# Kernel tuning notes

Measured on AMD Instinct MI355X. Metric: run time of the kernel, lower is better.

## Reference

```python
import jax, jax.numpy as jnp
import numpy as np

B, N, F_DIM = 64, 4096, 64
K_SLOTS, D, N_ITERS = 8, 64, 3
EPS = 1e-8
LN_EPS = 1e-5  # torch LayerNorm default


def layernorm(x, g, b):
    mu = jnp.mean(x, axis=-1, keepdims=True)
    var = jnp.mean(jnp.square(x - mu), axis=-1, keepdims=True)
    return (x - mu) * jax.lax.rsqrt(var + LN_EPS) * g + b


def gru_cell(x, h, w_ih, w_hh, b_ih, b_hh):
    # torch.nn.GRUCell semantics; weights are [3D, D] with gate order r, z, n
    gi = x @ w_ih.T + b_ih
    gh = h @ w_hh.T + b_hh
    i_r, i_z, i_n = jnp.split(gi, 3, axis=-1)
    h_r, h_z, h_n = jnp.split(gh, 3, axis=-1)
    r = jax.nn.sigmoid(i_r + h_r)
    z = jax.nn.sigmoid(i_z + h_z)
    n = jnp.tanh(i_n + r * h_n)
    return (1.0 - z) * n + z * h


def setup_inputs() -> dict:
    key = jax.random.key(0)
    ks = jax.random.split(key, 16)
    f32 = jnp.float32
    s = 0.05  # small init scale for weights
    return {
        "inputs": jax.random.normal(ks[0], (B, N, F_DIM), f32),
        "slots_noise": jax.random.normal(ks[1], (B, K_SLOTS, D), f32),
        "slots_mu": jax.random.normal(ks[2], (1, 1, D), f32) * s,
        "slots_log_sigma": jax.random.normal(ks[3], (1, 1, D), f32) * s,
        "Wq": jax.random.normal(ks[4], (D, D), f32) * s,
        "Wk": jax.random.normal(ks[5], (D, F_DIM), f32) * s,
        "Wv": jax.random.normal(ks[6], (D, F_DIM), f32) * s,
        "gru_w_ih": jax.random.normal(ks[7], (3 * D, D), f32) * s,
        "gru_w_hh": jax.random.normal(ks[8], (3 * D, D), f32) * s,
        "gru_b_ih": jnp.zeros((3 * D,), f32),
        "gru_b_hh": jnp.zeros((3 * D,), f32),
        "mlp_w1": jax.random.normal(ks[9], (2 * D, D), f32) * s,
        "mlp_b1": jnp.zeros((2 * D,), f32),
        "mlp_w2": jax.random.normal(ks[10], (D, 2 * D), f32) * s,
        "mlp_b2": jnp.zeros((D,), f32),
        "ln_in_g": jnp.ones((F_DIM,), f32), "ln_in_b": jnp.zeros((F_DIM,), f32),
        "ln_slots_g": jnp.ones((D,), f32), "ln_slots_b": jnp.zeros((D,), f32),
        "ln_mlp_g": jnp.ones((D,), f32), "ln_mlp_b": jnp.zeros((D,), f32),
    }


def reference(inputs, slots_noise, slots_mu, slots_log_sigma, Wq, Wk, Wv,
              gru_w_ih, gru_w_hh, gru_b_ih, gru_b_hh,
              mlp_w1, mlp_b1, mlp_w2, mlp_b2,
              ln_in_g, ln_in_b, ln_slots_g, ln_slots_b, ln_mlp_g, ln_mlp_b):
    x = layernorm(inputs, ln_in_g, ln_in_b)          # [B, N, F]
    k = jnp.einsum('bnf,df->bnd', x, Wk)             # [B, N, D]
    v = jnp.einsum('bnf,df->bnd', x, Wv)             # [B, N, D]

    slots = slots_mu + jnp.exp(slots_log_sigma) * slots_noise  # [B, K, D]
    scale = D ** -0.5

    for _ in range(N_ITERS):
        slots_prev = slots
        s_n = layernorm(slots, ln_slots_g, ln_slots_b)
        q = jnp.einsum('bkd,ed->bke', s_n, Wq)                  # [B, K, D]
        attn_logits = jnp.einsum('bnd,bkd->bnk', k, q) * scale  # [B, N, K]
        attn = jax.nn.softmax(attn_logits, axis=-1) + EPS       # softmax over slots
        attn = attn / jnp.sum(attn, axis=1, keepdims=True)      # renormalize over N
        updates = jnp.einsum('bnk,bnd->bkd', attn, v)           # [B, K, D]
        slots = gru_cell(updates.reshape(-1, D), slots_prev.reshape(-1, D),
                         gru_w_ih, gru_w_hh, gru_b_ih, gru_b_hh).reshape(B, K_SLOTS, D)
        h = layernorm(slots, ln_mlp_g, ln_mlp_b)
        h = jax.nn.relu(h @ mlp_w1.T + mlp_b1) @ mlp_w2.T + mlp_b2
        slots = slots + h
    return slots
```

## Files before the change

### kernel.cpp

```cpp
#include <hip/hip_runtime.h>
#include <math.h>

#define NN 4096
#define LN_EPS 1e-5f
#define EPS 1e-8f

typedef unsigned short ushortT;
typedef unsigned int uintT;
typedef __attribute__((ext_vector_type(8))) short short8;
typedef __attribute__((ext_vector_type(4))) float f32x4;
typedef __attribute__((ext_vector_type(2))) float f32x2;
typedef __attribute__((ext_vector_type(4))) unsigned short us4;

#define OFF_QU    0L
#define OFF_AP    98304L
#define OFF_CP    884736L
#define OFF_SLOTS 897024L
#define OFF_WIHT  995328L
#define OFF_WHHT  1007616L
#define OFF_W1T   1019904L
#define OFF_W2T   1028096L
#define OFF_WQT   1036288L
#define OFF_WVT   1040384L
#define OFF_CNT   1044480L
#define OFF_RDY   1044672L

__device__ __forceinline__ float wredsum(float v) {
#pragma unroll
  for (int off = 32; off > 0; off >>= 1) v += __shfl_xor(v, off);
  return v;
}

__device__ __forceinline__ ushortT f2bf(float f) {
  uintT b = __float_as_uint(f);
  b += 0x7fff + ((b >> 16) & 1);
  return (ushortT)(b >> 16);
}

__device__ __forceinline__ uintT pack2bf(float lo, float hi) {
  return (uintT)f2bf(lo) | ((uintT)f2bf(hi) << 16);
}

__device__ __forceinline__ void store2_coh(float* p, f32x2 v) {
  asm volatile("global_store_dwordx2 %0, %1, off sc0 sc1" :: "v"(p), "v"(v) : "memory");
}
__device__ __forceinline__ void store1f_coh(float* p, float v) {
  asm volatile("global_store_dword %0, %1, off sc0 sc1" :: "v"(p), "v"(v) : "memory");
}
__device__ __forceinline__ void store1u_coh(uintT* p, uintT v) {
  asm volatile("global_store_dword %0, %1, off sc0 sc1" :: "v"(p), "v"(v) : "memory");
}
__device__ __forceinline__ uintT load1u_coh(const uintT* p) {
  uintT r;
  asm volatile("global_load_dword %0, %1, off sc0 sc1\n\t"
               "s_waitcnt vmcnt(0)" : "=v"(r) : "v"(p) : "memory");
  return r;
}
__device__ __forceinline__ void drain_vm() {
  asm volatile("s_waitcnt vmcnt(0)" ::: "memory");
}
__device__ __forceinline__ void wait_lds() {
  asm volatile("s_waitcnt lgkmcnt(0)" ::: "memory");
}

__global__ __launch_bounds__(256) void k_prep(
    const float* __restrict__ w_ih, const float* __restrict__ w_hh,
    const float* __restrict__ w1, const float* __restrict__ w2,
    const float* __restrict__ Wq, const float* __restrict__ Wv,
    const float* __restrict__ Wk,
    const float* __restrict__ noise, const float* __restrict__ smu,
    const float* __restrict__ slsig,
    const float* __restrict__ g_sl, const float* __restrict__ b_sl,
    float* __restrict__ wihT, float* __restrict__ whhT,
    float* __restrict__ w1T, float* __restrict__ w2T, float* __restrict__ wqT,
    float* __restrict__ wvT, float* __restrict__ slotsV, uintT* __restrict__ qU,
    uintT* __restrict__ cnt, uintT* __restrict__ ready)
{
  const int tid = threadIdx.x;
  if (blockIdx.x >= 194) {
    __shared__ float SI[4][192];
    const int lane = tid & 63, wave = tid >> 6;
    const int bi = blockIdx.x - 194;
    const int row = bi * 4 + wave;
    const int b = row >> 3, ks = row & 7;
    float* Sw = SI[wave];

    float s0 = fmaf(expf(slsig[lane]), noise[row * 64 + lane], smu[lane]);
    slotsV[row * 64 + lane] = s0;

    float mu = wredsum(s0) * (1.f / 64.f);
    float dx = s0 - mu;
    float var = wredsum(dx * dx) * (1.f / 64.f);
    float sn = dx * rsqrtf(var + LN_EPS) * g_sl[lane] + b_sl[lane];
    Sw[lane] = sn;
    float qe = 0.f;
#pragma unroll 16
    for (int d = 0; d < 64; ++d) qe = fmaf(Sw[d], Wq[lane * 64 + d], qe);
    Sw[64 + lane] = qe;
    float qp = 0.f;
#pragma unroll 16
    for (int e = 0; e < 64; ++e) qp = fmaf(Sw[64 + e], Wk[e * 64 + lane], qp);
    Sw[128 + lane] = qp * 0.125f;
    if (lane < 32) {
      const int kb = lane >> 4, lrow = (lane >> 2) & 3, j2 = lane & 3;
      const int fA = kb * 32 + lrow * 8 + 2 * j2;
      uintT u = pack2bf(Sw[128 + fA], Sw[128 + fA + 1]);
      qU[((b * 2 + kb) * 64 + lrow * 16 + ks) * 4 + j2] = u;
#pragma unroll
      for (int v = 0; v < 3; ++v)
        qU[v * 32768 + ((b * 2 + kb) * 64 + lrow * 16 + 8 + ks) * 4 + j2] = 0u;
    }
    return;
  }

  int idx = blockIdx.x * 256 + tid;
  if (idx < 12288) {
    int j = idx >> 6, f = idx & 63;
    wihT[f * 192 + j] = w_ih[idx];
  } else if (idx < 24576) {
    int i = idx - 12288; int j = i >> 6, f = i & 63;
    whhT[f * 192 + j] = w_hh[i];
  } else if (idx < 32768) {
    int i = idx - 24576; int j = i >> 6, f = i & 63;
    w1T[f * 128 + j] = w1[i];
  } else if (idx < 40960) {
    int i = idx - 32768; int d = i >> 7, j = i & 127;
    w2T[j * 64 + d] = w2[i];
  } else if (idx < 45056) {
    int i = idx - 40960; int e = i >> 6, d = i & 63;
    wqT[d * 64 + e] = Wq[i];
  } else if (idx < 49152) {
    int i = idx - 45056; int d = i >> 6, f = i & 63;
    wvT[f * 64 + d] = Wv[i];
  } else if (idx < 49344) {
    cnt[idx - 49152] = 0u;
  } else if (idx < 49408) {
    ready[idx - 49344] = 0u;
  }
}

__global__ __launch_bounds__(256, 2) void k_attn(
    const float* __restrict__ inp,
    const float* __restrict__ g_in, const float* __restrict__ b_in,
    uintT* __restrict__ qU,
    float* __restrict__ accPart, float* __restrict__ colPart,
    uintT* __restrict__ cnt, uintT* __restrict__ ready,
    float* __restrict__ slotsV,
    const float* __restrict__ wihT, const float* __restrict__ whhT,
    const float* __restrict__ w1T, const float* __restrict__ w2T,
    const float* __restrict__ wqT, const float* __restrict__ Wk,
    const float* __restrict__ wvT,
    const float* __restrict__ b_ih, const float* __restrict__ b_hh,
    const float* __restrict__ mb1, const float* __restrict__ mb2,
    const float* __restrict__ g_ml, const float* __restrict__ b_ml,
    const float* __restrict__ g_sl, const float* __restrict__ b_sl,
    float* __restrict__ dout)
{
  __shared__ __align__(16) ushortT XW[4][4096];
  __shared__ int lastFlag;
  const int tid = threadIdx.x;
  const int lane = tid & 63;
  const int wave = tid >> 6;
  const int l15 = lane & 15, q = lane >> 4;
  const int b = blockIdx.x >> 3;
  const int e = blockIdx.x & 7;

  ushortT* xT = &XW[wave][0];

  short8 kA0[4][2], kA1[4][2];
  {
    const float4 g4 = *(const float4*)&g_in[l15 << 2];
    const float4 b4 = *(const float4*)&b_in[l15 << 2];
#pragma unroll
    for (int ch = 0; ch < 2; ++ch) {
      const int chunk = (e << 3) + (ch << 2) + wave;
      const float* rowbase = inp + (((long)b * NN + (chunk << 6)) << 6);
#pragma unroll
      for (int pass = 0; pass < 16; ++pass) {
        const int row = (pass << 2) + q;
        float4 x = *(const float4*)&rowbase[(row << 6) + (l15 << 2)];
        float s = x.x + x.y + x.z + x.w;
        s += __shfl_xor(s, 1); s += __shfl_xor(s, 2);
        s += __shfl_xor(s, 4); s += __shfl_xor(s, 8);
        const float mu = s * (1.f / 64.f);
        float4 dx = {x.x - mu, x.y - mu, x.z - mu, x.w - mu};
        float ss = dx.x * dx.x + dx.y * dx.y + dx.z * dx.z + dx.w * dx.w;
        ss += __shfl_xor(ss, 1); ss += __shfl_xor(ss, 2);
        ss += __shfl_xor(ss, 4); ss += __shfl_xor(ss, 8);
        const float rs = rsqrtf(ss * (1.f / 64.f) + LN_EPS);
        us4 p = {f2bf(dx.x * rs * g4.x + b4.x), f2bf(dx.y * rs * g4.y + b4.y),
                 f2bf(dx.z * rs * g4.z + b4.z), f2bf(dx.w * rs * g4.w + b4.w)};
        *(us4*)&xT[((((row >> 4) * 2 + (l15 >> 3)) << 6)
                    + (((l15 & 7) >> 1) << 4) + (row & 15)) * 8
                   + ((l15 & 1) << 2)] = p;
      }
      wait_lds();
#pragma unroll
      for (int mt = 0; mt < 4; ++mt)
#pragma unroll
        for (int kb = 0; kb < 2; ++kb) {
          short8 v = *(const short8*)&xT[((mt * 2 + kb) * 64 + lane) << 3];
          if (ch) kA1[mt][kb] = v; else kA0[mt][kb] = v;
        }
      wait_lds();
    }
  }

  for (int it = 0; it < 3; ++it) {
    if (it > 0) {
      if (tid == 0) {
        while (load1u_coh(&ready[b]) < (uintT)it) __builtin_amdgcn_s_sleep(2);
      }
      __syncthreads();
    }

    const uintT* qIt = qU + it * 32768;
    short8 qB[2];
#pragma unroll
    for (int kb = 0; kb < 2; ++kb)
      qB[kb] = *(const short8*)&qIt[((b * 2 + kb) * 64 + lane) * 4];

    f32x4 accP[4];
#pragma unroll
    for (int nt = 0; nt < 4; ++nt) accP[nt] = (f32x4){0.f, 0.f, 0.f, 0.f};
    float csum = 0.f;

#pragma unroll
    for (int ch = 0; ch < 2; ++ch) {
      f32x4 accL[4];
#pragma unroll
      for (int mt = 0; mt < 4; ++mt) {
        const short8 a0 = ch ? kA1[mt][0] : kA0[mt][0];
        const short8 a1 = ch ? kA1[mt][1] : kA0[mt][1];
        accL[mt] = (f32x4){0.f, 0.f, 0.f, 0.f};
        accL[mt] = __builtin_amdgcn_mfma_f32_16x16x32_bf16(a0, qB[0], accL[mt], 0, 0, 0);
        accL[mt] = __builtin_amdgcn_mfma_f32_16x16x32_bf16(a1, qB[1], accL[mt], 0, 0, 0);
      }

      {
        const int h = ((lane >> 5) << 2) | (((lane & 15) >> 3) << 1) | ((lane >> 4) & 1);
        const int jp = lane & 7;
        const int lpA = (((lane >> 4) & 1) << 3) + (((lane & 15) >> 3) << 4);
#pragma unroll
        for (int mt = 0; mt < 4; ++mt)
#pragma unroll
          for (int kb = 0; kb < 2; ++kb) {
            const int fb = (kb * 4 + ((lane >> 5) << 1) + (mt >> 1)) << 9;
            const int lm = lpA + ((mt & 1) << 5);
            const short8 src8 = ch ? kA1[mt][kb] : kA0[mt][kb];
            const ushortT* src = (const ushortT*)&src8;
#pragma unroll
            for (int j = 0; j < 8; ++j)
              xT[fb + (((lm + j) ^ h) << 3) + jp] = src[j];
          }
      }
      short8 vB[4][2];
#pragma unroll
      for (int nt = 0; nt < 4; ++nt)
#pragma unroll
        for (int ks = 0; ks < 2; ++ks) {
          const int frag = nt * 2 + ks;
          const int hr = ((nt & 1) << 2) | (((lane >> 4) & 1) << 1) | ((lane >> 3) & 1);
          vB[nt][ks] = *(const short8*)&xT[(frag << 9) + ((lane ^ hr) << 3)];
        }

      ushortT* attnF = &XW[wave][0];
#pragma unroll
      for (int mt = 0; mt < 4; ++mt) {
        float av[4];
#pragma unroll
        for (int r = 0; r < 4; ++r) {
          float lv = accL[mt][r];
          float mx = lv;
          mx = fmaxf(mx, __shfl_xor(mx, 1));
          mx = fmaxf(mx, __shfl_xor(mx, 2));
          mx = fmaxf(mx, __shfl_xor(mx, 4));
          float ev = __expf(lv - mx);
          float sv = ev;
          sv += __shfl_xor(sv, 1); sv += __shfl_xor(sv, 2); sv += __shfl_xor(sv, 4);
          float a = ev * (1.f / sv) + EPS;
          av[r] = a;
          csum += a;
        }
        us4 p = {f2bf(av[0]), f2bf(av[1]), f2bf(av[2]), f2bf(av[3])};
        *(us4*)&attnF[((((mt >> 1) << 6) + (((mt & 1) * 2 + (q >> 1)) << 4)
                        + l15) << 3) + ((q & 1) << 2)] = p;
      }

      short8 pA0 = *(const short8*)&attnF[(0 * 64 + lane) << 3];
      short8 pA1 = *(const short8*)&attnF[(1 * 64 + lane) << 3];

#pragma unroll
      for (int nt = 0; nt < 4; ++nt) {
        accP[nt] = __builtin_amdgcn_mfma_f32_16x16x32_bf16(pA0, vB[nt][0], accP[nt], 0, 0, 0);
        accP[nt] = __builtin_amdgcn_mfma_f32_16x16x32_bf16(pA1, vB[nt][1], accP[nt], 0, 0, 0);
      }
    }

    csum += __shfl_xor(csum, 16);
    csum += __shfl_xor(csum, 32);

    float* accLw = (float*)&XW[wave][1024];
    float* colLw = (float*)&XW[wave][2048];
    if (q < 2) {
#pragma unroll
      for (int nt = 0; nt < 4; ++nt)
#pragma unroll
        for (int r = 0; r < 4; ++r)
          accLw[(q * 4 + r) * 64 + nt * 16 + l15] = accP[nt][r];
    }
    if (q == 0 && l15 < 8) colLw[l15] = csum;
    __syncthreads();

    float* apIt = accPart + ((long)(it * 64 + b) * 8 + e) * 512;
    float* cpIt = colPart + ((long)(it * 64 + b) * 8 + e) * 8;
    {
      const int o = tid * 2;
      f32x2 s;
#pragma unroll
      for (int r = 0; r < 2; ++r) {
        const int oo = o + r;
        s[r] = *((float*)&XW[0][1024] + oo) + *((float*)&XW[1][1024] + oo)
             + *((float*)&XW[2][1024] + oo) + *((float*)&XW[3][1024] + oo);
      }
      store2_coh(&apIt[o], s);
    }
    if (tid < 8) {
      float s = *((float*)&XW[0][2048] + tid) + *((float*)&XW[1][2048] + tid)
              + *((float*)&XW[2][2048] + tid) + *((float*)&XW[3][2048] + tid);
      store1f_coh(&cpIt[tid], s);
    }

    drain_vm();
    __syncthreads();
    if (tid == 0) lastFlag = (atomicAdd(&cnt[it * 64 + b], 1u) == 7u);
    __syncthreads();

    if (lastFlag) {
      const int ks0 = wave, ks1 = wave + 4;
      const int row0 = b * 8 + ks0, row1 = b * 8 + ks1;
      const float* apB = accPart + (long)(it * 64 + b) * 8 * 512;
      const float* cpB = colPart + (long)(it * 64 + b) * 8 * 8;
      const float* slIt = slotsV + it * 32768;

      float csv0 = 0.f, csv1 = 0.f, t0 = 0.f, t1 = 0.f;
#pragma unroll
      for (int ee = 0; ee < 8; ++ee) {
        csv0 += cpB[ee * 8 + ks0];
        csv1 += cpB[ee * 8 + ks1];
        t0 += apB[ee * 512 + ks0 * 64 + lane];
        t1 += apB[ee * 512 + ks1 * 64 + lane];
      }
      t0 /= csv0; t1 /= csv1;
      const float h0 = slIt[row0 * 64 + lane];
      const float h1 = slIt[row1 * 64 + lane];

      float* S = (float*)&XW[wave][0];

      S[256 + lane] = t0; S[320 + lane] = t1;
      float u0 = 0.f, u1 = 0.f;
#pragma unroll 4
      for (int f = 0; f < 64; ++f) {
        const float wv = wvT[f * 64 + lane];
        u0 = fmaf(S[256 + f], wv, u0);
        u1 = fmaf(S[320 + f], wv, u1);
      }

      S[lane] = u0; S[64 + lane] = u1; S[128 + lane] = h0; S[192 + lane] = h1;

      float gir0 = b_ih[lane], giz0 = b_ih[64 + lane], gin0 = b_ih[128 + lane];
      float ghr0 = b_hh[lane], ghz0 = b_hh[64 + lane], ghn0 = b_hh[128 + lane];
      float gir1 = gir0, giz1 = giz0, gin1 = gin0;
      float ghr1 = ghr0, ghz1 = ghz0, ghn1 = ghn0;
#pragma unroll 4
      for (int f = 0; f < 64; ++f) {
        const float wr = wihT[f * 192 + lane], wz = wihT[f * 192 + 64 + lane],
                    wn = wihT[f * 192 + 128 + lane];
        const float vr = whhT[f * 192 + lane], vz = whhT[f * 192 + 64 + lane],
                    vn = whhT[f * 192 + 128 + lane];
        const float a0 = S[f], a1 = S[64 + f], c0 = S[128 + f], c1 = S[192 + f];
        gir0 = fmaf(a0, wr, gir0); gir1 = fmaf(a1, wr, gir1);
        giz0 = fmaf(a0, wz, giz0); giz1 = fmaf(a1, wz, giz1);
        gin0 = fmaf(a0, wn, gin0); gin1 = fmaf(a1, wn, gin1);
        ghr0 = fmaf(c0, vr, ghr0); ghr1 = fmaf(c1, vr, ghr1);
        ghz0 = fmaf(c0, vz, ghz0); ghz1 = fmaf(c1, vz, ghz1);
        ghn0 = fmaf(c0, vn, ghn0); ghn1 = fmaf(c1, vn, ghn1);
      }
      const float r0 = 1.f / (1.f + expf(-(gir0 + ghr0)));
      const float z0 = 1.f / (1.f + expf(-(giz0 + ghz0)));
      const float n0 = tanhf(fmaf(r0, ghn0, gin0));
      const float hn0 = (1.f - z0) * n0 + z0 * h0;
      const float r1 = 1.f / (1.f + expf(-(gir1 + ghr1)));
      const float z1 = 1.f / (1.f + expf(-(giz1 + ghz1)));
      const float n1 = tanhf(fmaf(r1, ghn1, gin1));
      const float hn1 = (1.f - z1) * n1 + z1 * h1;

      float mu0 = wredsum(hn0) * (1.f / 64.f);
      float dx0 = hn0 - mu0;
      float va0 = wredsum(dx0 * dx0) * (1.f / 64.f);
      const float ln0 = dx0 * rsqrtf(va0 + LN_EPS) * g_ml[lane] + b_ml[lane];
      float mu1 = wredsum(hn1) * (1.f / 64.f);
      float dx1 = hn1 - mu1;
      float va1 = wredsum(dx1 * dx1) * (1.f / 64.f);
      const float ln1 = dx1 * rsqrtf(va1 + LN_EPS) * g_ml[lane] + b_ml[lane];
      S[256 + lane] = ln0; S[320 + lane] = ln1;

      float h1a0 = mb1[lane], h1b0 = mb1[64 + lane];
      float h1a1 = h1a0, h1b1 = h1b0;
#pragma unroll 4
      for (int f = 0; f < 64; ++f) {
        const float wa = w1T[f * 128 + lane], wb = w1T[f * 128 + 64 + lane];
        const float l0 = S[256 + f], l1 = S[320 + f];
        h1a0 = fmaf(l0, wa, h1a0); h1a1 = fmaf(l1, wa, h1a1);
        h1b0 = fmaf(l0, wb, h1b0); h1b1 = fmaf(l1, wb, h1b1);
      }
      h1a0 = fmaxf(h1a0, 0.f); h1b0 = fmaxf(h1b0, 0.f);
      h1a1 = fmaxf(h1a1, 0.f); h1b1 = fmaxf(h1b1, 0.f);
      S[lane] = h1a0; S[64 + lane] = h1b0;
      S[128 + lane] = h1a1; S[192 + lane] = h1b1;

      float o0 = mb2[lane], o1 = mb2[lane];
#pragma unroll 4
      for (int j = 0; j < 128; ++j) {
        const float w2v = w2T[j * 64 + lane];
        o0 = fmaf(S[j], w2v, o0);
        o1 = fmaf(S[128 + j], w2v, o1);
      }
      const float sn0 = hn0 + o0;
      const float sn1 = hn1 + o1;

      if (it == 2) {
        dout[row0 * 64 + lane] = sn0;
        dout[row1 * 64 + lane] = sn1;
      } else {
        float* slN = slotsV + (it + 1) * 32768;
        store1f_coh(&slN[row0 * 64 + lane], sn0);
        store1f_coh(&slN[row1 * 64 + lane], sn1);

        float m20 = wredsum(sn0) * (1.f / 64.f);
        float d20 = sn0 - m20;
        float v20 = wredsum(d20 * d20) * (1.f / 64.f);
        const float sq0 = d20 * rsqrtf(v20 + LN_EPS) * g_sl[lane] + b_sl[lane];
        float m21 = wredsum(sn1) * (1.f / 64.f);
        float d21 = sn1 - m21;
        float v21 = wredsum(d21 * d21) * (1.f / 64.f);
        const float sq1 = d21 * rsqrtf(v21 + LN_EPS) * g_sl[lane] + b_sl[lane];
        S[256 + lane] = sq0; S[320 + lane] = sq1;
        float qe0 = 0.f, qe1 = 0.f;
#pragma unroll 8
        for (int d = 0; d < 64; ++d) {
          const float wq = wqT[d * 64 + lane];
          qe0 = fmaf(S[256 + d], wq, qe0);
          qe1 = fmaf(S[320 + d], wq, qe1);
        }
        S[256 + lane] = qe0; S[320 + lane] = qe1;
        float qp0 = 0.f, qp1 = 0.f;
#pragma unroll 8
        for (int e2 = 0; e2 < 64; ++e2) {
          const float wk = Wk[e2 * 64 + lane];
          qp0 = fmaf(S[256 + e2], wk, qp0);
          qp1 = fmaf(S[320 + e2], wk, qp1);
        }
        S[384 + lane] = qp0 * 0.125f;
        S[448 + lane] = qp1 * 0.125f;
        {
          uintT* qN = qU + (it + 1) * 32768;
          const int rr = lane >> 5, L5 = lane & 31;
          const int kb = L5 >> 4, lrow = (L5 >> 2) & 3, j2 = L5 & 3;
          const int fA = kb * 32 + lrow * 8 + 2 * j2;
          const int ksr = rr ? ks1 : ks0;
          uintT u = pack2bf(S[384 + rr * 64 + fA], S[384 + rr * 64 + fA + 1]);
          store1u_coh(&qN[((b * 2 + kb) * 64 + lrow * 16 + ksr) * 4 + j2], u);
        }
        drain_vm();
        __syncthreads();
        if (tid == 0) atomicAdd(&ready[b], 1u);
      }
    }
  }
}

extern "C" void kernel_launch(void* const* d_in, const int* in_sizes, int n_in,
                              void* d_out, int out_size, void* d_ws, size_t ws_size,
                              hipStream_t stream) {
  const float* inp   = (const float*)d_in[0];
  const float* noise = (const float*)d_in[1];
  const float* smu   = (const float*)d_in[2];
  const float* slsig = (const float*)d_in[3];
  const float* Wq    = (const float*)d_in[4];
  const float* Wk    = (const float*)d_in[5];
  const float* Wv    = (const float*)d_in[6];
  const float* w_ih  = (const float*)d_in[7];
  const float* w_hh  = (const float*)d_in[8];
  const float* b_ih  = (const float*)d_in[9];
  const float* b_hh  = (const float*)d_in[10];
  const float* w1    = (const float*)d_in[11];
  const float* b1    = (const float*)d_in[12];
  const float* w2    = (const float*)d_in[13];
  const float* b2    = (const float*)d_in[14];
  const float* g_in  = (const float*)d_in[15];
  const float* bi_in = (const float*)d_in[16];
  const float* g_sl  = (const float*)d_in[17];
  const float* bi_sl = (const float*)d_in[18];
  const float* g_ml  = (const float*)d_in[19];
  const float* bi_ml = (const float*)d_in[20];

  float* ws      = (float*)d_ws;
  uintT* qU      = (uintT*)(ws + OFF_QU);
  float* ap      = ws + OFF_AP;
  float* cp      = ws + OFF_CP;
  float* sl      = ws + OFF_SLOTS;
  float* wihT    = ws + OFF_WIHT;
  float* whhT    = ws + OFF_WHHT;
  float* w1T     = ws + OFF_W1T;
  float* w2T     = ws + OFF_W2T;
  float* wqT     = ws + OFF_WQT;
  float* wvT     = ws + OFF_WVT;
  uintT* cnt     = (uintT*)(ws + OFF_CNT);
  uintT* rdy     = (uintT*)(ws + OFF_RDY);

  k_prep<<<322, 256, 0, stream>>>(w_ih, w_hh, w1, w2, Wq, Wv, Wk,
                                  noise, smu, slsig, g_sl, bi_sl,
                                  wihT, whhT, w1T, w2T, wqT, wvT,
                                  sl, qU, cnt, rdy);
  k_attn<<<512, 256, 0, stream>>>(inp, g_in, bi_in, qU, ap, cp, cnt, rdy, sl,
                                  wihT, whhT, w1T, w2T, wqT, Wk, wvT,
                                  b_ih, b_hh, b1, b2, g_ml, bi_ml, g_sl, bi_sl,
                                  (float*)d_out);
}
```

Baseline: 244.8 us.

## Replicate slot update in every block instead of last-block election and ready flag

```diff
diff --git a/kernel.cpp b/kernel.cpp
--- a/kernel.cpp
+++ b/kernel.cpp
@@ -12,18 +12,15 @@
 typedef __attribute__((ext_vector_type(2))) float f32x2;
 typedef __attribute__((ext_vector_type(4))) unsigned short us4;
 
-#define OFF_QU    0L
-#define OFF_AP    98304L
-#define OFF_CP    884736L
-#define OFF_SLOTS 897024L
-#define OFF_WIHT  995328L
-#define OFF_WHHT  1007616L
-#define OFF_W1T   1019904L
-#define OFF_W2T   1028096L
-#define OFF_WQT   1036288L
-#define OFF_WVT   1040384L
-#define OFF_CNT   1044480L
-#define OFF_RDY   1044672L
+#define OFF_AP    0L
+#define OFF_CP    786432L
+#define OFF_WIHP  798720L
+#define OFF_WHHP  815104L
+#define OFF_W1P   831488L
+#define OFF_W2T   839680L
+#define OFF_WQT   847872L
+#define OFF_WVT   851968L
+#define OFF_CNT   856064L
 
 __device__ __forceinline__ float wredsum(float v) {
 #pragma unroll
@@ -37,17 +34,10 @@
   return (ushortT)(b >> 16);
 }
 
-__device__ __forceinline__ uintT pack2bf(float lo, float hi) {
-  return (uintT)f2bf(lo) | ((uintT)f2bf(hi) << 16);
-}
-
 __device__ __forceinline__ void store2_coh(float* p, f32x2 v) {
   asm volatile("global_store_dwordx2 %0, %1, off sc0 sc1" :: "v"(p), "v"(v) : "memory");
 }
 __device__ __forceinline__ void store1f_coh(float* p, float v) {
-  asm volatile("global_store_dword %0, %1, off sc0 sc1" :: "v"(p), "v"(v) : "memory");
-}
-__device__ __forceinline__ void store1u_coh(uintT* p, uintT v) {
   asm volatile("global_store_dword %0, %1, off sc0 sc1" :: "v"(p), "v"(v) : "memory");
 }
 __device__ __forceinline__ uintT load1u_coh(const uintT* p) {
@@ -67,87 +57,45 @@
     const float* __restrict__ w_ih, const float* __restrict__ w_hh,
     const float* __restrict__ w1, const float* __restrict__ w2,
     const float* __restrict__ Wq, const float* __restrict__ Wv,
-    const float* __restrict__ Wk,
-    const float* __restrict__ noise, const float* __restrict__ smu,
-    const float* __restrict__ slsig,
-    const float* __restrict__ g_sl, const float* __restrict__ b_sl,
-    float* __restrict__ wihT, float* __restrict__ whhT,
-    float* __restrict__ w1T, float* __restrict__ w2T, float* __restrict__ wqT,
-    float* __restrict__ wvT, float* __restrict__ slotsV, uintT* __restrict__ qU,
-    uintT* __restrict__ cnt, uintT* __restrict__ ready)
+    float* __restrict__ wihP, float* __restrict__ whhP,
+    float* __restrict__ w1P, float* __restrict__ w2T, float* __restrict__ wqT,
+    float* __restrict__ wvT, uintT* __restrict__ cnt)
 {
-  const int tid = threadIdx.x;
-  if (blockIdx.x >= 194) {
-    __shared__ float SI[4][192];
-    const int lane = tid & 63, wave = tid >> 6;
-    const int bi = blockIdx.x - 194;
-    const int row = bi * 4 + wave;
-    const int b = row >> 3, ks = row & 7;
-    float* Sw = SI[wave];
-
-    float s0 = fmaf(expf(slsig[lane]), noise[row * 64 + lane], smu[lane]);
-    slotsV[row * 64 + lane] = s0;
-
-    float mu = wredsum(s0) * (1.f / 64.f);
-    float dx = s0 - mu;
-    float var = wredsum(dx * dx) * (1.f / 64.f);
-    float sn = dx * rsqrtf(var + LN_EPS) * g_sl[lane] + b_sl[lane];
-    Sw[lane] = sn;
-    float qe = 0.f;
-#pragma unroll 16
-    for (int d = 0; d < 64; ++d) qe = fmaf(Sw[d], Wq[lane * 64 + d], qe);
-    Sw[64 + lane] = qe;
-    float qp = 0.f;
-#pragma unroll 16
-    for (int e = 0; e < 64; ++e) qp = fmaf(Sw[64 + e], Wk[e * 64 + lane], qp);
-    Sw[128 + lane] = qp * 0.125f;
-    if (lane < 32) {
-      const int kb = lane >> 4, lrow = (lane >> 2) & 3, j2 = lane & 3;
-      const int fA = kb * 32 + lrow * 8 + 2 * j2;
-      uintT u = pack2bf(Sw[128 + fA], Sw[128 + fA + 1]);
-      qU[((b * 2 + kb) * 64 + lrow * 16 + ks) * 4 + j2] = u;
-#pragma unroll
-      for (int v = 0; v < 3; ++v)
-        qU[v * 32768 + ((b * 2 + kb) * 64 + lrow * 16 + 8 + ks) * 4 + j2] = 0u;
-    }
-    return;
-  }
-
-  int idx = blockIdx.x * 256 + tid;
-  if (idx < 12288) {
-    int j = idx >> 6, f = idx & 63;
-    wihT[f * 192 + j] = w_ih[idx];
-  } else if (idx < 24576) {
-    int i = idx - 12288; int j = i >> 6, f = i & 63;
-    whhT[f * 192 + j] = w_hh[i];
+  int idx = blockIdx.x * 256 + threadIdx.x;
+  if (idx < 16384) {
+    int g = idx & 3, l = (idx >> 2) & 63, f = idx >> 8;
+    wihP[idx] = (g < 3) ? w_ih[(g * 64 + l) * 64 + f] : 0.f;
   } else if (idx < 32768) {
-    int i = idx - 24576; int j = i >> 6, f = i & 63;
-    w1T[f * 128 + j] = w1[i];
+    int i = idx - 16384;
+    int g = i & 3, l = (i >> 2) & 63, f = i >> 8;
+    whhP[i] = (g < 3) ? w_hh[(g * 64 + l) * 64 + f] : 0.f;
   } else if (idx < 40960) {
-    int i = idx - 32768; int d = i >> 7, j = i & 127;
+    int i = idx - 32768;
+    int g = i & 1, l = (i >> 1) & 63, f = i >> 7;
+    w1P[i] = w1[(g * 64 + l) * 64 + f];
+  } else if (idx < 49152) {
+    int i = idx - 40960; int d = i >> 7, j = i & 127;
     w2T[j * 64 + d] = w2[i];
-  } else if (idx < 45056) {
-    int i = idx - 40960; int e = i >> 6, d = i & 63;
+  } else if (idx < 53248) {
+    int i = idx - 49152; int e = i >> 6, d = i & 63;
     wqT[d * 64 + e] = Wq[i];
-  } else if (idx < 49152) {
-    int i = idx - 45056; int d = i >> 6, f = i & 63;
+  } else if (idx < 57344) {
+    int i = idx - 53248; int d = i >> 6, f = i & 63;
     wvT[f * 64 + d] = Wv[i];
-  } else if (idx < 49344) {
-    cnt[idx - 49152] = 0u;
-  } else if (idx < 49408) {
-    ready[idx - 49344] = 0u;
+  } else if (idx < 57536) {
+    cnt[idx - 57344] = 0u;
   }
 }
 
 __global__ __launch_bounds__(256, 2) void k_attn(
     const float* __restrict__ inp,
     const float* __restrict__ g_in, const float* __restrict__ b_in,
-    uintT* __restrict__ qU,
+    const float* __restrict__ noise, const float* __restrict__ smu,
+    const float* __restrict__ slsig,
     float* __restrict__ accPart, float* __restrict__ colPart,
-    uintT* __restrict__ cnt, uintT* __restrict__ ready,
-    float* __restrict__ slotsV,
-    const float* __restrict__ wihT, const float* __restrict__ whhT,
-    const float* __restrict__ w1T, const float* __restrict__ w2T,
+    uintT* __restrict__ cnt,
+    const float* __restrict__ wihP, const float* __restrict__ whhP,
+    const float* __restrict__ w1P, const float* __restrict__ w2T,
     const float* __restrict__ wqT, const float* __restrict__ Wk,
     const float* __restrict__ wvT,
     const float* __restrict__ b_ih, const float* __restrict__ b_hh,
@@ -157,7 +105,6 @@
     float* __restrict__ dout)
 {
   __shared__ __align__(16) ushortT XW[4][4096];
-  __shared__ int lastFlag;
   const int tid = threadIdx.x;
   const int lane = tid & 63;
   const int wave = tid >> 6;
@@ -166,6 +113,12 @@
   const int e = blockIdx.x & 7;
 
   ushortT* xT = &XW[wave][0];
+
+  const int row0 = b * 8 + wave, row1 = row0 + 4;
+
+  const float es = expf(slsig[lane]);
+  float h0p = fmaf(es, noise[row0 * 64 + lane], smu[lane]);
+  float h1p = fmaf(es, noise[row1 * 64 + lane], smu[lane]);
 
   short8 kA0[4][2], kA1[4][2];
   {
@@ -206,20 +159,56 @@
     }
   }
 
+  short8 qB[2];
+
+  auto slots_to_qB = [&](float sv0, float sv1) {
+    float* S = (float*)&XW[wave][0];
+    float* qS = (float*)&XW[0][1024];
+    float m0 = wredsum(sv0) * (1.f / 64.f);
+    float d0 = sv0 - m0;
+    float v0 = wredsum(d0 * d0) * (1.f / 64.f);
+    const float sq0 = d0 * rsqrtf(v0 + LN_EPS) * g_sl[lane] + b_sl[lane];
+    float m1 = wredsum(sv1) * (1.f / 64.f);
+    float d1 = sv1 - m1;
+    float v1 = wredsum(d1 * d1) * (1.f / 64.f);
+    const float sq1 = d1 * rsqrtf(v1 + LN_EPS) * g_sl[lane] + b_sl[lane];
+    S[lane] = sq0; S[64 + lane] = sq1;
+    float qe0 = 0.f, qe1 = 0.f;
+#pragma unroll 8
+    for (int d = 0; d < 64; ++d) {
+      const float wq = wqT[d * 64 + lane];
+      qe0 = fmaf(S[d], wq, qe0);
+      qe1 = fmaf(S[64 + d], wq, qe1);
+    }
+    S[128 + lane] = qe0; S[192 + lane] = qe1;
+    float qp0 = 0.f, qp1 = 0.f;
+#pragma unroll 8
+    for (int e2 = 0; e2 < 64; ++e2) {
+      const float wk = Wk[e2 * 64 + lane];
+      qp0 = fmaf(S[128 + e2], wk, qp0);
+      qp1 = fmaf(S[192 + e2], wk, qp1);
+    }
+    __syncthreads();
+    qS[wave * 64 + lane] = qp0 * 0.125f;
+    qS[(wave + 4) * 64 + lane] = qp1 * 0.125f;
+    __syncthreads();
+#pragma unroll
+    for (int kb = 0; kb < 2; ++kb) {
+      ushortT tmp[8];
+#pragma unroll
+      for (int j = 0; j < 8; ++j) {
+        const int col = lane & 15;
+        float v = (col < 8) ? qS[col * 64 + kb * 32 + ((lane >> 4) << 3) + j] : 0.f;
+        tmp[j] = f2bf(v);
+      }
+      qB[kb] = *(short8*)tmp;
+    }
+    __syncthreads();
+  };
+
+  slots_to_qB(h0p, h1p);
+
   for (int it = 0; it < 3; ++it) {
-    if (it > 0) {
-      if (tid == 0) {
-        while (load1u_coh(&ready[b]) < (uintT)it) __builtin_amdgcn_s_sleep(2);
-      }
-      __syncthreads();
-    }
-
-    const uintT* qIt = qU + it * 32768;
-    short8 qB[2];
-#pragma unroll
-    for (int kb = 0; kb < 2; ++kb)
-      qB[kb] = *(const short8*)&qIt[((b * 2 + kb) * 64 + lane) * 4];
-
     f32x4 accP[4];
 #pragma unroll
     for (int nt = 0; nt < 4; ++nt) accP[nt] = (f32x4){0.f, 0.f, 0.f, 0.f};
@@ -333,150 +322,111 @@
 
     drain_vm();
     __syncthreads();
-    if (tid == 0) lastFlag = (atomicAdd(&cnt[it * 64 + b], 1u) == 7u);
-    __syncthreads();
-
-    if (lastFlag) {
-      const int ks0 = wave, ks1 = wave + 4;
-      const int row0 = b * 8 + ks0, row1 = b * 8 + ks1;
-      const float* apB = accPart + (long)(it * 64 + b) * 8 * 512;
-      const float* cpB = colPart + (long)(it * 64 + b) * 8 * 8;
-      const float* slIt = slotsV + it * 32768;
-
-      float csv0 = 0.f, csv1 = 0.f, t0 = 0.f, t1 = 0.f;
-#pragma unroll
-      for (int ee = 0; ee < 8; ++ee) {
-        csv0 += cpB[ee * 8 + ks0];
-        csv1 += cpB[ee * 8 + ks1];
-        t0 += apB[ee * 512 + ks0 * 64 + lane];
-        t1 += apB[ee * 512 + ks1 * 64 + lane];
-      }
-      t0 /= csv0; t1 /= csv1;
-      const float h0 = slIt[row0 * 64 + lane];
-      const float h1 = slIt[row1 * 64 + lane];
-
-      float* S = (float*)&XW[wave][0];
-
-      S[256 + lane] = t0; S[320 + lane] = t1;
-      float u0 = 0.f, u1 = 0.f;
+    if (tid == 0) atomicAdd(&cnt[it * 64 + b], 1u);
+
+    if (it == 2 && e != 0) return;
+
+    if (tid == 0) {
+      while (load1u_coh(&cnt[it * 64 + b]) < 8u) __builtin_amdgcn_s_sleep(2);
+    }
+    __syncthreads();
+
+    const float* apB = accPart + (long)(it * 64 + b) * 8 * 512;
+    const float* cpB = colPart + (long)(it * 64 + b) * 8 * 8;
+
+    float csv0 = 0.f, csv1 = 0.f, t0 = 0.f, t1 = 0.f;
+#pragma unroll
+    for (int ee = 0; ee < 8; ++ee) {
+      csv0 += cpB[ee * 8 + wave];
+      csv1 += cpB[ee * 8 + wave + 4];
+      t0 += apB[ee * 512 + wave * 64 + lane];
+      t1 += apB[ee * 512 + (wave + 4) * 64 + lane];
+    }
+    t0 /= csv0; t1 /= csv1;
+    const float h0 = h0p, h1 = h1p;
+
+    float* S = (float*)&XW[wave][0];
+
+    S[256 + lane] = t0; S[320 + lane] = t1;
+    float u0 = 0.f, u1 = 0.f;
 #pragma unroll 4
-      for (int f = 0; f < 64; ++f) {
-        const float wv = wvT[f * 64 + lane];
-        u0 = fmaf(S[256 + f], wv, u0);
-        u1 = fmaf(S[320 + f], wv, u1);
-      }
-
-      S[lane] = u0; S[64 + lane] = u1; S[128 + lane] = h0; S[192 + lane] = h1;
-
-      float gir0 = b_ih[lane], giz0 = b_ih[64 + lane], gin0 = b_ih[128 + lane];
-      float ghr0 = b_hh[lane], ghz0 = b_hh[64 + lane], ghn0 = b_hh[128 + lane];
-      float gir1 = gir0, giz1 = giz0, gin1 = gin0;
-      float ghr1 = ghr0, ghz1 = ghz0, ghn1 = ghn0;
+    for (int f = 0; f < 64; ++f) {
+      const float wv = wvT[f * 64 + lane];
+      u0 = fmaf(S[256 + f], wv, u0);
+      u1 = fmaf(S[320 + f], wv, u1);
+    }
+
+    S[lane] = u0; S[64 + lane] = u1; S[128 + lane] = h0; S[192 + lane] = h1;
+
+    float gir0 = b_ih[lane], giz0 = b_ih[64 + lane], gin0 = b_ih[128 + lane];
+    float ghr0 = b_hh[lane], ghz0 = b_hh[64 + lane], ghn0 = b_hh[128 + lane];
+    float gir1 = gir0, giz1 = giz0, gin1 = gin0;
+    float ghr1 = ghr0, ghz1 = ghz0, ghn1 = ghn0;
+    const float4* wihP4 = (const float4*)wihP;
+    const float4* whhP4 = (const float4*)whhP;
+#pragma unroll 8
+    for (int f = 0; f < 64; ++f) {
+      const float4 wi = wihP4[f * 64 + lane];
+      const float4 wh = whhP4[f * 64 + lane];
+      const float a0 = S[f], a1 = S[64 + f], c0 = S[128 + f], c1 = S[192 + f];
+      gir0 = fmaf(a0, wi.x, gir0); gir1 = fmaf(a1, wi.x, gir1);
+      giz0 = fmaf(a0, wi.y, giz0); giz1 = fmaf(a1, wi.y, giz1);
+      gin0 = fmaf(a0, wi.z, gin0); gin1 = fmaf(a1, wi.z, gin1);
+      ghr0 = fmaf(c0, wh.x, ghr0); ghr1 = fmaf(c1, wh.x, ghr1);
+      ghz0 = fmaf(c0, wh.y, ghz0); ghz1 = fmaf(c1, wh.y, ghz1);
+      ghn0 = fmaf(c0, wh.z, ghn0); ghn1 = fmaf(c1, wh.z, ghn1);
+    }
+    const float r0 = 1.f / (1.f + expf(-(gir0 + ghr0)));
+    const float z0 = 1.f / (1.f + expf(-(giz0 + ghz0)));
+    const float n0 = tanhf(fmaf(r0, ghn0, gin0));
+    const float hn0 = (1.f - z0) * n0 + z0 * h0;
+    const float r1 = 1.f / (1.f + expf(-(gir1 + ghr1)));
+    const float z1 = 1.f / (1.f + expf(-(giz1 + ghz1)));
+    const float n1 = tanhf(fmaf(r1, ghn1, gin1));
+    const float hn1 = (1.f - z1) * n1 + z1 * h1;
+
+    float mu0 = wredsum(hn0) * (1.f / 64.f);
+    float dx0 = hn0 - mu0;
+    float va0 = wredsum(dx0 * dx0) * (1.f / 64.f);
+    const float ln0 = dx0 * rsqrtf(va0 + LN_EPS) * g_ml[lane] + b_ml[lane];
+    float mu1 = wredsum(hn1) * (1.f / 64.f);
+    float dx1 = hn1 - mu1;
+    float va1 = wredsum(dx1 * dx1) * (1.f / 64.f);
+    const float ln1 = dx1 * rsqrtf(va1 + LN_EPS) * g_ml[lane] + b_ml[lane];
+    S[256 + lane] = ln0; S[320 + lane] = ln1;
+
+    float h1a0 = mb1[lane], h1b0 = mb1[64 + lane];
+    float h1a1 = h1a0, h1b1 = h1b0;
+    const f32x2* w1P2 = (const f32x2*)w1P;
+#pragma unroll 8
+    for (int f = 0; f < 64; ++f) {
+      const f32x2 w = w1P2[f * 64 + lane];
+      const float l0 = S[256 + f], l1 = S[320 + f];
+      h1a0 = fmaf(l0, w.x, h1a0); h1a1 = fmaf(l1, w.x, h1a1);
+      h1b0 = fmaf(l0, w.y, h1b0); h1b1 = fmaf(l1, w.y, h1b1);
+    }
+    h1a0 = fmaxf(h1a0, 0.f); h1b0 = fmaxf(h1b0, 0.f);
+    h1a1 = fmaxf(h1a1, 0.f); h1b1 = fmaxf(h1b1, 0.f);
+    S[lane] = h1a0; S[64 + lane] = h1b0;
+    S[128 + lane] = h1a1; S[192 + lane] = h1b1;
+
+    float o0 = mb2[lane], o1 = mb2[lane];
 #pragma unroll 4
-      for (int f = 0; f < 64; ++f) {
-        const float wr = wihT[f * 192 + lane], wz = wihT[f * 192 + 64 + lane],
-                    wn = wihT[f * 192 + 128 + lane];
-        const float vr = whhT[f * 192 + lane], vz = whhT[f * 192 + 64 + lane],
-                    vn = whhT[f * 192 + 128 + lane];
-        const float a0 = S[f], a1 = S[64 + f], c0 = S[128 + f], c1 = S[192 + f];
-        gir0 = fmaf(a0, wr, gir0); gir1 = fmaf(a1, wr, gir1);
-        giz0 = fmaf(a0, wz, giz0); giz1 = fmaf(a1, wz, giz1);
-        gin0 = fmaf(a0, wn, gin0); gin1 = fmaf(a1, wn, gin1);
-        ghr0 = fmaf(c0, vr, ghr0); ghr1 = fmaf(c1, vr, ghr1);
-        ghz0 = fmaf(c0, vz, ghz0); ghz1 = fmaf(c1, vz, ghz1);
-        ghn0 = fmaf(c0, vn, ghn0); ghn1 = fmaf(c1, vn, ghn1);
-      }
-      const float r0 = 1.f / (1.f + expf(-(gir0 + ghr0)));
-      const float z0 = 1.f / (1.f + expf(-(giz0 + ghz0)));
-      const float n0 = tanhf(fmaf(r0, ghn0, gin0));
-      const float hn0 = (1.f - z0) * n0 + z0 * h0;
-      const float r1 = 1.f / (1.f + expf(-(gir1 + ghr1)));
-      const float z1 = 1.f / (1.f + expf(-(giz1 + ghz1)));
-      const float n1 = tanhf(fmaf(r1, ghn1, gin1));
-      const float hn1 = (1.f - z1) * n1 + z1 * h1;
-
-      float mu0 = wredsum(hn0) * (1.f / 64.f);
-      float dx0 = hn0 - mu0;
-      float va0 = wredsum(dx0 * dx0) * (1.f / 64.f);
-      const float ln0 = dx0 * rsqrtf(va0 + LN_EPS) * g_ml[lane] + b_ml[lane];
-      float mu1 = wredsum(hn1) * (1.f / 64.f);
-      float dx1 = hn1 - mu1;
-      float va1 = wredsum(dx1 * dx1) * (1.f / 64.f);
-      const float ln1 = dx1 * rsqrtf(va1 + LN_EPS) * g_ml[lane] + b_ml[lane];
-      S[256 + lane] = ln0; S[320 + lane] = ln1;
-
-      float h1a0 = mb1[lane], h1b0 = mb1[64 + lane];
-      float h1a1 = h1a0, h1b1 = h1b0;
-#pragma unroll 4
-      for (int f = 0; f < 64; ++f) {
-        const float wa = w1T[f * 128 + lane], wb = w1T[f * 128 + 64 + lane];
-        const float l0 = S[256 + f], l1 = S[320 + f];
-        h1a0 = fmaf(l0, wa, h1a0); h1a1 = fmaf(l1, wa, h1a1);
-        h1b0 = fmaf(l0, wb, h1b0); h1b1 = fmaf(l1, wb, h1b1);
-      }
-      h1a0 = fmaxf(h1a0, 0.f); h1b0 = fmaxf(h1b0, 0.f);
-      h1a1 = fmaxf(h1a1, 0.f); h1b1 = fmaxf(h1b1, 0.f);
-      S[lane] = h1a0; S[64 + lane] = h1b0;
-      S[128 + lane] = h1a1; S[192 + lane] = h1b1;
-
-      float o0 = mb2[lane], o1 = mb2[lane];
-#pragma unroll 4
-      for (int j = 0; j < 128; ++j) {
-        const float w2v = w2T[j * 64 + lane];
-        o0 = fmaf(S[j], w2v, o0);
-        o1 = fmaf(S[128 + j], w2v, o1);
-      }
-      const float sn0 = hn0 + o0;
-      const float sn1 = hn1 + o1;
-
-      if (it == 2) {
-        dout[row0 * 64 + lane] = sn0;
-        dout[row1 * 64 + lane] = sn1;
-      } else {
-        float* slN = slotsV + (it + 1) * 32768;
-        store1f_coh(&slN[row0 * 64 + lane], sn0);
-        store1f_coh(&slN[row1 * 64 + lane], sn1);
-
-        float m20 = wredsum(sn0) * (1.f / 64.f);
-        float d20 = sn0 - m20;
-        float v20 = wredsum(d20 * d20) * (1.f / 64.f);
-        const float sq0 = d20 * rsqrtf(v20 + LN_EPS) * g_sl[lane] + b_sl[lane];
-        float m21 = wredsum(sn1) * (1.f / 64.f);
-        float d21 = sn1 - m21;
-        float v21 = wredsum(d21 * d21) * (1.f / 64.f);
-        const float sq1 = d21 * rsqrtf(v21 + LN_EPS) * g_sl[lane] + b_sl[lane];
-        S[256 + lane] = sq0; S[320 + lane] = sq1;
-        float qe0 = 0.f, qe1 = 0.f;
-#pragma unroll 8
-        for (int d = 0; d < 64; ++d) {
-          const float wq = wqT[d * 64 + lane];
-          qe0 = fmaf(S[256 + d], wq, qe0);
-          qe1 = fmaf(S[320 + d], wq, qe1);
-        }
-        S[256 + lane] = qe0; S[320 + lane] = qe1;
-        float qp0 = 0.f, qp1 = 0.f;
-#pragma unroll 8
-        for (int e2 = 0; e2 < 64; ++e2) {
-          const float wk = Wk[e2 * 64 + lane];
-          qp0 = fmaf(S[256 + e2], wk, qp0);
-          qp1 = fmaf(S[320 + e2], wk, qp1);
-        }
-        S[384 + lane] = qp0 * 0.125f;
-        S[448 + lane] = qp1 * 0.125f;
-        {
-          uintT* qN = qU + (it + 1) * 32768;
-          const int rr = lane >> 5, L5 = lane & 31;
-          const int kb = L5 >> 4, lrow = (L5 >> 2) & 3, j2 = L5 & 3;
-          const int fA = kb * 32 + lrow * 8 + 2 * j2;
-          const int ksr = rr ? ks1 : ks0;
-          uintT u = pack2bf(S[384 + rr * 64 + fA], S[384 + rr * 64 + fA + 1]);
-          store1u_coh(&qN[((b * 2 + kb) * 64 + lrow * 16 + ksr) * 4 + j2], u);
-        }
-        drain_vm();
-        __syncthreads();
-        if (tid == 0) atomicAdd(&ready[b], 1u);
-      }
-    }
+    for (int j = 0; j < 128; ++j) {
+      const float w2v = w2T[j * 64 + lane];
+      o0 = fmaf(S[j], w2v, o0);
+      o1 = fmaf(S[128 + j], w2v, o1);
+    }
+    const float sn0 = hn0 + o0;
+    const float sn1 = hn1 + o1;
+
+    if (it == 2) {
+      dout[row0 * 64 + lane] = sn0;
+      dout[row1 * 64 + lane] = sn1;
+      return;
+    }
+    h0p = sn0; h1p = sn1;
+    slots_to_qB(sn0, sn1);
   }
 }
 
@@ -506,25 +456,21 @@
   const float* bi_ml = (const float*)d_in[20];
 
   float* ws      = (float*)d_ws;
-  uintT* qU      = (uintT*)(ws + OFF_QU);
   float* ap      = ws + OFF_AP;
   float* cp      = ws + OFF_CP;
-  float* sl      = ws + OFF_SLOTS;
-  float* wihT    = ws + OFF_WIHT;
-  float* whhT    = ws + OFF_WHHT;
-  float* w1T     = ws + OFF_W1T;
+  float* wihP    = ws + OFF_WIHP;
+  float* whhP    = ws + OFF_WHHP;
+  float* w1P     = ws + OFF_W1P;
   float* w2T     = ws + OFF_W2T;
   float* wqT     = ws + OFF_WQT;
   float* wvT     = ws + OFF_WVT;
   uintT* cnt     = (uintT*)(ws + OFF_CNT);
-  uintT* rdy     = (uintT*)(ws + OFF_RDY);
-
-  k_prep<<<322, 256, 0, stream>>>(w_ih, w_hh, w1, w2, Wq, Wv, Wk,
-                                  noise, smu, slsig, g_sl, bi_sl,
-                                  wihT, whhT, w1T, w2T, wqT, wvT,
-                                  sl, qU, cnt, rdy);
-  k_attn<<<512, 256, 0, stream>>>(inp, g_in, bi_in, qU, ap, cp, cnt, rdy, sl,
-                                  wihT, whhT, w1T, w2T, wqT, Wk, wvT,
+
+  k_prep<<<225, 256, 0, stream>>>(w_ih, w_hh, w1, w2, Wq, Wv,
+                                  wihP, whhP, w1P, w2T, wqT, wvT, cnt);
+  k_attn<<<512, 256, 0, stream>>>(inp, g_in, bi_in, noise, smu, slsig,
+                                  ap, cp, cnt,
+                                  wihP, whhP, w1P, w2T, wqT, Wk, wvT,
                                   b_ih, b_hh, b1, b2, g_ml, bi_ml, g_sl, bi_sl,
                                   (float*)d_out);
 }
```

Result: slower. 250.3 us (+2.2%).
